# Optimization experiments

Measured on AMD Instinct MI355X. Metric: run time of the kernel, lower is better.

Reference implementation:

```python
import jax, jax.numpy as jnp
import numpy as np

B, H, S, D = 2, 16, 2048, 128


def setup_inputs() -> dict:
    key = jax.random.key(0)
    ks = jax.random.split(key, 11)
    s = 1.0 / np.sqrt(D)
    return {
        "query": jax.random.normal(ks[0], (B, H, S, D), dtype=jnp.float32),
        "key": jax.random.normal(ks[1], (B, H, S, D), dtype=jnp.float32),
        "value": jax.random.normal(ks[2], (B, H, S, D), dtype=jnp.float32),
        "Wq": jax.random.normal(ks[3], (D, D), dtype=jnp.float32) * s,
        "bq": jnp.zeros((D,), dtype=jnp.float32),
        "Wk": jax.random.normal(ks[4], (D, D), dtype=jnp.float32) * s,
        "bk": jnp.zeros((D,), dtype=jnp.float32),
        "Wv": jax.random.normal(ks[5], (D, D), dtype=jnp.float32) * s,
        "bv": jnp.zeros((D,), dtype=jnp.float32),
        "Wo": jax.random.normal(ks[6], (D, D), dtype=jnp.float32) * s,
        "bo": jnp.zeros((D,), dtype=jnp.float32),
    }


def reference(query, key, value, Wq, bq, Wk, bk, Wv, bv, Wo, bo):
    # Linear projections (torch Linear: x @ W^T + b) on last dim of [B,H,S,D]
    q = jnp.einsum("bhsd,ed->bhse", query, Wq) + bq
    k = jnp.einsum("bhsd,ed->bhse", key, Wk) + bk
    v = jnp.einsum("bhsd,ed->bhse", value, Wv) + bv
    scale = jnp.sqrt(jnp.asarray(D, dtype=q.dtype))
    q = q / scale
    qk = jnp.einsum("bhse,bhte->bhst", q, k)  # [B,H,S,S] scores
    attn = jax.nn.softmax(qk, axis=-1)
    # dropout_p = 0.0 -> identity
    out = jnp.einsum("bhst,bhtd->bhsd", attn, v)
    out = jnp.einsum("bhsd,ed->bhse", out, Wo) + bo
    return out
```

## Files before the change

kernel.cpp:

```cpp
#include <hip/hip_runtime.h>
#include <hip/hip_bf16.h>
#include <type_traits>
#include <math.h>

typedef __bf16 bf16x8 __attribute__((ext_vector_type(8)));
typedef float floatx4 __attribute__((ext_vector_type(4)));
typedef float floatx16 __attribute__((ext_vector_type(16)));

#define S_LEN 2048
#define D_DIM 128
#define NTOK (2 * 16 * 2048)
#define KVB 64
#define NKV (S_LEN / KVB)

template <typename TIN, typename TOUT>
__device__ __forceinline__ void proj_body4(
    const TIN* __restrict__ x, const float* __restrict__ W,
    const float* __restrict__ b, TOUT* __restrict__ y, float out_scale,
    int chunk0, __bf16 (*Wl)[128]) {
  const int tid = threadIdx.x;
  const int wave = tid >> 6, lane = tid & 63;
  const int g = lane >> 4, lr = lane & 15;

  for (int it = 0; it < 16; ++it) {
    int lin = it * 1024 + tid * 4;
    float4 w4 = *reinterpret_cast<const float4*>(W + lin);
    int r = lin >> 7, c = lin & 127;
    Wl[r][c]     = (__bf16)w4.x;
    Wl[r][c + 1] = (__bf16)w4.y;
    Wl[r][c + 2] = (__bf16)w4.z;
    Wl[r][c + 3] = (__bf16)w4.w;
  }
  __syncthreads();

  float be[8];
#pragma unroll
  for (int nt = 0; nt < 8; ++nt) be[nt] = b[nt * 16 + lr];

  for (int ch = 0; ch < 4; ++ch) {
    const int rbase = (chunk0 + ch) * 64;
    const int arow = rbase + wave * 16 + lr;

    floatx4 acc[8];
#pragma unroll
    for (int i = 0; i < 8; ++i) acc[i] = floatx4{0.f, 0.f, 0.f, 0.f};

#pragma unroll
    for (int kc = 0; kc < 4; ++kc) {
      bf16x8 af;
      const TIN* xp = x + (size_t)arow * D_DIM + kc * 32 + g * 8;
      if constexpr (std::is_same<TIN, float>::value) {
        float4 f0 = *reinterpret_cast<const float4*>(xp);
        float4 f1 = *reinterpret_cast<const float4*>(xp + 4);
        af[0] = (__bf16)f0.x; af[1] = (__bf16)f0.y;
        af[2] = (__bf16)f0.z; af[3] = (__bf16)f0.w;
        af[4] = (__bf16)f1.x; af[5] = (__bf16)f1.y;
        af[6] = (__bf16)f1.z; af[7] = (__bf16)f1.w;
      } else {
        af = *reinterpret_cast<const bf16x8*>(xp);
      }
#pragma unroll
      for (int nt = 0; nt < 8; ++nt) {
        bf16x8 wf = *reinterpret_cast<const bf16x8*>(&Wl[nt * 16 + lr][kc * 32 + g * 8]);
        acc[nt] = __builtin_amdgcn_mfma_f32_16x16x32_bf16(af, wf, acc[nt], 0, 0, 0);
      }
    }

#pragma unroll
    for (int nt = 0; nt < 8; ++nt) {
      int e = nt * 16 + lr;
#pragma unroll
      for (int j = 0; j < 4; ++j) {
        int row = rbase + wave * 16 + g * 4 + j;
        float val = (acc[nt][j] + be[nt]) * out_scale;
        y[(size_t)row * D_DIM + e] = (TOUT)val;
      }
    }
  }
}

__global__ __launch_bounds__(256) void qkv_proj_kernel(
    const float* __restrict__ xq, const float* __restrict__ xk,
    const float* __restrict__ xv, const float* __restrict__ Wq,
    const float* __restrict__ Wk, const float* __restrict__ Wv,
    const float* __restrict__ bq, const float* __restrict__ bk,
    const float* __restrict__ bv, __bf16* yq, __bf16* yk, __bf16* yv,
    float qscale) {
  __shared__ alignas(16) __bf16 Wl[128][128];
  const int which = blockIdx.y;
  const float* x = which == 0 ? xq : which == 1 ? xk : xv;
  const float* W = which == 0 ? Wq : which == 1 ? Wk : Wv;
  const float* b = which == 0 ? bq : which == 1 ? bk : bv;
  __bf16* y = which == 0 ? yq : which == 1 ? yk : yv;
  float sc = which == 0 ? qscale : 1.0f;
  proj_body4<float, __bf16>(x, W, b, y, sc, blockIdx.x * 4, Wl);
}

__global__ __launch_bounds__(256) void o_proj_kernel(
    const __bf16* __restrict__ x, const float* __restrict__ W,
    const float* __restrict__ b, float* __restrict__ y) {
  __shared__ alignas(16) __bf16 Wl[128][128];
  proj_body4<__bf16, float>(x, W, b, y, 1.0f, blockIdx.x * 4, Wl);
}

__device__ __forceinline__ unsigned swz(int row, unsigned byteoff) {
  return byteoff ^ (((unsigned)(row ^ (row >> 3)) & 7u) << 4);
}

__device__ __forceinline__ unsigned pack2(float lo, float hi) {
  union { __bf16 h[2]; unsigned u; } r;
  r.h[0] = (__bf16)lo; r.h[1] = (__bf16)hi;
  return r.u;
}

__global__ __launch_bounds__(256, 2) void attn_kernel(
    const __bf16* __restrict__ q, const __bf16* __restrict__ k,
    const __bf16* __restrict__ v, __bf16* __restrict__ o) {
  __shared__ alignas(16) unsigned char smem[65536];

  const int tid = threadIdx.x;
  const int wave = tid >> 6, lane = tid & 63;
  const int ql = lane & 31;
  const int h = lane >> 5;

  const int bh = blockIdx.x;
  const int qbase = blockIdx.y * 128;
  const __bf16* qp = q + (size_t)bh * S_LEN * D_DIM;
  const __bf16* kp = k + (size_t)bh * S_LEN * D_DIM;
  const __bf16* vp = v + (size_t)bh * S_LEN * D_DIM;
  __bf16* op = o + (size_t)bh * S_LEN * D_DIM;

  const int qrow = qbase + wave * 32 + ql;
  bf16x8 qf[8];
#pragma unroll
  for (int kc = 0; kc < 8; ++kc)
    qf[kc] = *reinterpret_cast<const bf16x8*>(
        qp + (size_t)qrow * D_DIM + kc * 16 + h * 8);

  floatx16 ot[4];
#pragma unroll
  for (int d = 0; d < 4; ++d)
#pragma unroll
    for (int r = 0; r < 16; ++r) ot[d][r] = 0.f;
  float m_r = -1e30f, l_r = 0.f;

  const int cc = tid & 15;
  const int pr = (tid >> 4) * 2;
  const int ce = cc * 8;

  unsigned Rk[4];
#pragma unroll
  for (int x = 0; x < 4; ++x)
    Rk[x] = (unsigned)(h * 1024) +
            (((unsigned)(ql * 16)) ^ ((unsigned)h << 4) ^ ((unsigned)x << 5));
  const unsigned Rv0 = 32768u + (unsigned)(h * 2048) +
                       (((unsigned)(ql * 16)) ^ (((unsigned)(ql >> 3)) << 4));
  const unsigned Rv1 = Rv0 ^ 64u;
  const unsigned kx = ((unsigned)(cc & 7)) << 4;
  const unsigned Wk0 = ((unsigned)(cc * 1024 + pr * 16)) ^ kx;
  const unsigned Wk1 = ((unsigned)(cc * 1024 + (pr + 1) * 16)) ^ kx;
  unsigned Wv_[8];
  {
    unsigned vbase = 32768u + (unsigned)((pr >> 3) * 2048 + ce * 16 + (pr & 7) * 2);
#pragma unroll
    for (int e = 0; e < 8; ++e)
      Wv_[e] = vbase | (((unsigned)e << 4) ^ kx);
  }

  {
    const __bf16* kr = kp + (size_t)pr * D_DIM + ce;
    const __bf16* vr = vp + (size_t)pr * D_DIM + ce;
    bf16x8 kA0 = *reinterpret_cast<const bf16x8*>(kr);
    bf16x8 kA1 = *reinterpret_cast<const bf16x8*>(kr + D_DIM);
    bf16x8 kB0 = *reinterpret_cast<const bf16x8*>(kr + 32 * D_DIM);
    bf16x8 kB1 = *reinterpret_cast<const bf16x8*>(kr + 33 * D_DIM);
    union { bf16x8 v8; unsigned short s[8]; } vA0, vA1, vB0, vB1;
    vA0.v8 = *reinterpret_cast<const bf16x8*>(vr);
    vA1.v8 = *reinterpret_cast<const bf16x8*>(vr + D_DIM);
    vB0.v8 = *reinterpret_cast<const bf16x8*>(vr + 32 * D_DIM);
    vB1.v8 = *reinterpret_cast<const bf16x8*>(vr + 33 * D_DIM);
    *reinterpret_cast<bf16x8*>(smem + Wk0) = kA0;
    *reinterpret_cast<bf16x8*>(smem + Wk1) = kA1;
    *reinterpret_cast<bf16x8*>(smem + Wk0 + 512u) = kB0;
    *reinterpret_cast<bf16x8*>(smem + Wk1 + 512u) = kB1;
#pragma unroll
    for (int e = 0; e < 8; ++e) {
      unsigned w0 = (unsigned)vA0.s[e] | ((unsigned)vA1.s[e] << 16);
      unsigned w1 = (unsigned)vB0.s[e] | ((unsigned)vB1.s[e] << 16);
      *reinterpret_cast<unsigned*>(smem + Wv_[e]) = w0;
      *reinterpret_cast<unsigned*>(smem + Wv_[e] + 8192u) = w1;
    }
  }

  const __bf16* krp = kp + ((size_t)KVB + pr) * D_DIM + ce;
  const __bf16* vrp = vp + ((size_t)KVB + pr) * D_DIM + ce;

#pragma unroll 2
  for (int t = 0; t < NKV; ++t) {
    const unsigned cb = (unsigned)(t & 1) * 16384u;
    const bool hn = (t + 1 < NKV);

    __syncthreads();

    bf16x8 kA0, kA1, kB0, kB1;
    union { bf16x8 v8; unsigned short s[8]; } vA0, vA1, vB0, vB1;
    if (hn) {
      kA0 = *reinterpret_cast<const bf16x8*>(krp);
      kA1 = *reinterpret_cast<const bf16x8*>(krp + D_DIM);
      kB0 = *reinterpret_cast<const bf16x8*>(krp + 32 * D_DIM);
      kB1 = *reinterpret_cast<const bf16x8*>(krp + 33 * D_DIM);
      vA0.v8 = *reinterpret_cast<const bf16x8*>(vrp);
      vA1.v8 = *reinterpret_cast<const bf16x8*>(vrp + D_DIM);
      vB0.v8 = *reinterpret_cast<const bf16x8*>(vrp + 32 * D_DIM);
      vB1.v8 = *reinterpret_cast<const bf16x8*>(vrp + 33 * D_DIM);
      krp += (size_t)KVB * D_DIM;
      vrp += (size_t)KVB * D_DIM;
    }

    floatx16 st[2];
#pragma unroll
    for (int kvh = 0; kvh < 2; ++kvh)
#pragma unroll
      for (int r = 0; r < 16; ++r) st[kvh][r] = 0.f;
    __builtin_amdgcn_s_setprio(1);
#pragma unroll
    for (int kc = 0; kc < 8; ++kc) {
      bf16x8 kf0 = *reinterpret_cast<const bf16x8*>(
          smem + cb + Rk[kc & 3] + (unsigned)(kc * 2048));
      bf16x8 kf1 = *reinterpret_cast<const bf16x8*>(
          smem + cb + Rk[kc & 3] + (unsigned)(kc * 2048 + 512));
      st[0] = __builtin_amdgcn_mfma_f32_32x32x16_bf16(kf0, qf[kc], st[0], 0, 0, 0);
      st[1] = __builtin_amdgcn_mfma_f32_32x32x16_bf16(kf1, qf[kc], st[1], 0, 0, 0);
    }
    __builtin_amdgcn_s_setprio(0);

    float t8[8];
#pragma unroll
    for (int i = 0; i < 8; ++i)
      t8[i] = fmaxf(fmaxf(st[0][i], st[0][i + 8]), fmaxf(st[1][i], st[1][i + 8]));
    float pmax = fmaxf(fmaxf(fmaxf(t8[0], t8[4]), fmaxf(t8[1], t8[5])),
                       fmaxf(fmaxf(t8[2], t8[6]), fmaxf(t8[3], t8[7])));
    pmax = fmaxf(pmax, __shfl_xor(pmax, 32));
    if (!__all(pmax - m_r <= 8.0f)) {
      float mnew = fmaxf(m_r, pmax);
      float sc_f = __builtin_amdgcn_exp2f(m_r - mnew);
      m_r = mnew;
      l_r *= sc_f;
#pragma unroll
      for (int d = 0; d < 4; ++d)
#pragma unroll
        for (int r = 0; r < 16; ++r) ot[d][r] *= sc_f;
    }
#pragma unroll
    for (int kvh = 0; kvh < 2; ++kvh)
#pragma unroll
      for (int r = 0; r < 16; ++r)
        st[kvh][r] = __builtin_amdgcn_exp2f(st[kvh][r] - m_r);
    float s8[8];
#pragma unroll
    for (int i = 0; i < 8; ++i)
      s8[i] = (st[0][i] + st[0][i + 8]) + (st[1][i] + st[1][i + 8]);
    float psum = ((s8[0] + s8[4]) + (s8[1] + s8[5])) +
                 ((s8[2] + s8[6]) + (s8[3] + s8[7]));
    psum += __shfl_xor(psum, 32);
    l_r += psum;

#pragma unroll
    for (int ks = 0; ks < 4; ++ks) {
      const int kvh = ks >> 1;
      const int r2a = (2 * ks) & 3;
      const int r2b = r2a + 1;
      unsigned ua0 = pack2(st[kvh][r2a * 4 + 0], st[kvh][r2a * 4 + 1]);
      unsigned ua1 = pack2(st[kvh][r2a * 4 + 2], st[kvh][r2a * 4 + 3]);
      unsigned ub0 = pack2(st[kvh][r2b * 4 + 0], st[kvh][r2b * 4 + 1]);
      unsigned ub1 = pack2(st[kvh][r2b * 4 + 2], st[kvh][r2b * 4 + 3]);
      union { unsigned u[4]; bf16x8 v8; } pw;
#if __has_builtin(__builtin_amdgcn_permlane32_swap)
      {
        auto r0 = __builtin_amdgcn_permlane32_swap(ua0, ub0, false, false);
        auto r1 = __builtin_amdgcn_permlane32_swap(ua1, ub1, false, false);
        pw.u[0] = r0[0];
        pw.u[1] = r1[0];
        pw.u[2] = r0[1];
        pw.u[3] = r1[1];
      }
#else
      {
        unsigned a0x = __shfl_xor(ua0, 32), a1x = __shfl_xor(ua1, 32);
        unsigned b0x = __shfl_xor(ub0, 32), b1x = __shfl_xor(ub1, 32);
        pw.u[0] = h ? b0x : ua0;
        pw.u[1] = h ? b1x : ua1;
        pw.u[2] = h ? ub0 : a0x;
        pw.u[3] = h ? ub1 : a1x;
      }
#endif
      __builtin_amdgcn_s_setprio(1);
#pragma unroll
      for (int db = 0; db < 4; ++db) {
        const unsigned base = (db & 1) ? Rv1 : Rv0;
        bf16x8 vf = *reinterpret_cast<const bf16x8*>(
            smem + cb + base + (unsigned)(ks * 4096 + db * 512));
        ot[db] = __builtin_amdgcn_mfma_f32_32x32x16_bf16(vf, pw.v8, ot[db], 0, 0, 0);
      }
      __builtin_amdgcn_s_setprio(0);
    }

    if (hn) {
      const unsigned nb = cb ^ 16384u;
      *reinterpret_cast<bf16x8*>(smem + nb + Wk0) = kA0;
      *reinterpret_cast<bf16x8*>(smem + nb + Wk1) = kA1;
      *reinterpret_cast<bf16x8*>(smem + nb + Wk0 + 512u) = kB0;
      *reinterpret_cast<bf16x8*>(smem + nb + Wk1 + 512u) = kB1;
#pragma unroll
      for (int e = 0; e < 8; ++e) {
        unsigned w0 = (unsigned)vA0.s[e] | ((unsigned)vA1.s[e] << 16);
        unsigned w1 = (unsigned)vB0.s[e] | ((unsigned)vB1.s[e] << 16);
        *reinterpret_cast<unsigned*>(smem + nb + Wv_[e]) = w0;
        *reinterpret_cast<unsigned*>(smem + nb + Wv_[e] + 8192u) = w1;
      }
    }
  }

  __syncthreads();
  const float inv_l = 1.0f / l_r;
  const int qloc = wave * 32 + ql;
#pragma unroll
  for (int db = 0; db < 4; ++db)
#pragma unroll
    for (int r = 0; r < 16; ++r) {
      int d = db * 32 + (r & 3) + 8 * (r >> 2) + 4 * h;
      *reinterpret_cast<__bf16*>(smem + swz(qloc, qloc * 256u + d * 2u)) =
          (__bf16)(ot[db][r] * inv_l);
    }
  __syncthreads();
#pragma unroll
  for (int it = 0; it < 8; ++it) {
    int r = tid >> 1;
    int c = (tid & 1) * 64 + it * 8;
    bf16x8 val = *reinterpret_cast<const bf16x8*>(smem + swz(r, r * 256u + c * 2u));
    *reinterpret_cast<bf16x8*>(op + (size_t)(qbase + r) * D_DIM + c) = val;
  }
}

extern "C" void kernel_launch(void* const* d_in, const int* in_sizes, int n_in,
                              void* d_out, int out_size, void* d_ws, size_t ws_size,
                              hipStream_t stream) {
  const float* query = (const float*)d_in[0];
  const float* key_  = (const float*)d_in[1];
  const float* value = (const float*)d_in[2];
  const float* Wq = (const float*)d_in[3];
  const float* bq = (const float*)d_in[4];
  const float* Wk = (const float*)d_in[5];
  const float* bk = (const float*)d_in[6];
  const float* Wv = (const float*)d_in[7];
  const float* bv = (const float*)d_in[8];
  const float* Wo = (const float*)d_in[9];
  const float* bo = (const float*)d_in[10];

  __bf16* vws = (__bf16*)d_ws;
  __bf16* aws = vws + (size_t)NTOK * D_DIM;
  __bf16* qws = (__bf16*)d_out;
  __bf16* kws = qws + (size_t)NTOK * D_DIM;

  const float qscale = 0.1275174490036f;

  qkv_proj_kernel<<<dim3(NTOK / 256, 3), dim3(256), 0, stream>>>(
      query, key_, value, Wq, Wk, Wv, bq, bk, bv, qws, kws, vws, qscale);

  attn_kernel<<<dim3(32, 16), dim3(256), 0, stream>>>(qws, kws, vws, aws);

  o_proj_kernel<<<NTOK / 256, dim3(256), 0, stream>>>(aws, Wo, bo, (float*)d_out);
}
```

Before: 132.3 us.

## Split attention over two KV halves and merge partials inside output projection

Adds a split-KV attention kernel in which each block handles half of the key/value sequence. It writes fp32 normalized partial outputs plus log-sum-exp values, and the grid doubles to 1024 blocks with smaller shared memory and a higher occupancy target. A new output-projection kernel merges the two partials with softmax weights before the Wo matmul, fusing the combine step into it. This raises parallelism over the 256 CUs but adds fp32 partial traffic (two 32 MB buffers written and read). The path is used only when the workspace is large enough, otherwise the old path runs.

```diff
diff --git a/kernel.cpp b/kernel.cpp
--- a/kernel.cpp
+++ b/kernel.cpp
@@ -12,6 +12,8 @@
 #define NTOK (2 * 16 * 2048)
 #define KVB 64
 #define NKV (S_LEN / KVB)
+#define KVB_S 32
+#define NKV_S 32
 
 template <typename TIN, typename TOUT>
 __device__ __forceinline__ void proj_body4(
@@ -103,6 +105,80 @@
   proj_body4<__bf16, float>(x, W, b, y, 1.0f, blockIdx.x * 4, Wl);
 }
 
+__global__ __launch_bounds__(256) void o_proj_merge_kernel(
+    const float* __restrict__ p0, const float* __restrict__ p1,
+    const float* __restrict__ g0, const float* __restrict__ g1,
+    const float* __restrict__ W, const float* __restrict__ b,
+    float* __restrict__ y) {
+  __shared__ alignas(16) __bf16 Wl[128][128];
+  const int tid = threadIdx.x;
+  const int wave = tid >> 6, lane = tid & 63;
+  const int g = lane >> 4, lr = lane & 15;
+
+  for (int it = 0; it < 16; ++it) {
+    int lin = it * 1024 + tid * 4;
+    float4 w4 = *reinterpret_cast<const float4*>(W + lin);
+    int r = lin >> 7, c = lin & 127;
+    Wl[r][c]     = (__bf16)w4.x;
+    Wl[r][c + 1] = (__bf16)w4.y;
+    Wl[r][c + 2] = (__bf16)w4.z;
+    Wl[r][c + 3] = (__bf16)w4.w;
+  }
+  __syncthreads();
+
+  float be[8];
+#pragma unroll
+  for (int nt = 0; nt < 8; ++nt) be[nt] = b[nt * 16 + lr];
+
+  for (int ch = 0; ch < 4; ++ch) {
+    const int rbase = (blockIdx.x * 4 + ch) * 64;
+    const int arow = rbase + wave * 16 + lr;
+
+    const float ga = g0[arow], gb = g1[arow];
+    const float e2 = __builtin_amdgcn_exp2f(gb - ga);
+    const float w0 = 1.0f / (1.0f + e2);
+    const float w1 = 1.0f - w0;
+
+    floatx4 acc[8];
+#pragma unroll
+    for (int i = 0; i < 8; ++i) acc[i] = floatx4{0.f, 0.f, 0.f, 0.f};
+
+#pragma unroll
+    for (int kc = 0; kc < 4; ++kc) {
+      const float* xp0 = p0 + (size_t)arow * D_DIM + kc * 32 + g * 8;
+      const float* xp1 = p1 + (size_t)arow * D_DIM + kc * 32 + g * 8;
+      float4 a0 = *reinterpret_cast<const float4*>(xp0);
+      float4 a1 = *reinterpret_cast<const float4*>(xp0 + 4);
+      float4 c0 = *reinterpret_cast<const float4*>(xp1);
+      float4 c1 = *reinterpret_cast<const float4*>(xp1 + 4);
+      bf16x8 af;
+      af[0] = (__bf16)(w0 * a0.x + w1 * c0.x);
+      af[1] = (__bf16)(w0 * a0.y + w1 * c0.y);
+      af[2] = (__bf16)(w0 * a0.z + w1 * c0.z);
+      af[3] = (__bf16)(w0 * a0.w + w1 * c0.w);
+      af[4] = (__bf16)(w0 * a1.x + w1 * c1.x);
+      af[5] = (__bf16)(w0 * a1.y + w1 * c1.y);
+      af[6] = (__bf16)(w0 * a1.z + w1 * c1.z);
+      af[7] = (__bf16)(w0 * a1.w + w1 * c1.w);
+#pragma unroll
+      for (int nt = 0; nt < 8; ++nt) {
+        bf16x8 wf = *reinterpret_cast<const bf16x8*>(&Wl[nt * 16 + lr][kc * 32 + g * 8]);
+        acc[nt] = __builtin_amdgcn_mfma_f32_16x16x32_bf16(af, wf, acc[nt], 0, 0, 0);
+      }
+    }
+
+#pragma unroll
+    for (int nt = 0; nt < 8; ++nt) {
+      int e = nt * 16 + lr;
+#pragma unroll
+      for (int j = 0; j < 4; ++j) {
+        int row = rbase + wave * 16 + g * 4 + j;
+        y[(size_t)row * D_DIM + e] = acc[nt][j] + be[nt];
+      }
+    }
+  }
+}
+
 __device__ __forceinline__ unsigned swz(int row, unsigned byteoff) {
   return byteoff ^ (((unsigned)(row ^ (row >> 3)) & 7u) << 4);
 }
@@ -111,6 +187,225 @@
   union { __bf16 h[2]; unsigned u; } r;
   r.h[0] = (__bf16)lo; r.h[1] = (__bf16)hi;
   return r.u;
+}
+
+__global__ __launch_bounds__(256, 4) void attn_split_kernel(
+    const __bf16* __restrict__ q, const __bf16* __restrict__ k,
+    const __bf16* __restrict__ v, float* __restrict__ part0,
+    float* __restrict__ part1, float* __restrict__ g0w,
+    float* __restrict__ g1w) {
+  __shared__ alignas(16) unsigned char smem[32768];
+
+  const int tid = threadIdx.x;
+  const int wave = tid >> 6, lane = tid & 63;
+  const int ql = lane & 31;
+  const int h = lane >> 5;
+
+  const int bh = blockIdx.x;
+  const int qbase = blockIdx.y * 128;
+  const int half = blockIdx.z;
+  float* part = half ? part1 : part0;
+  float* gw = half ? g1w : g0w;
+
+  const __bf16* qp = q + (size_t)bh * S_LEN * D_DIM;
+  const __bf16* kp = k + (size_t)bh * S_LEN * D_DIM + (size_t)half * 1024 * D_DIM;
+  const __bf16* vp = v + (size_t)bh * S_LEN * D_DIM + (size_t)half * 1024 * D_DIM;
+
+  const int qrow = qbase + wave * 32 + ql;
+  bf16x8 qf[8];
+#pragma unroll
+  for (int kc = 0; kc < 8; ++kc)
+    qf[kc] = *reinterpret_cast<const bf16x8*>(
+        qp + (size_t)qrow * D_DIM + kc * 16 + h * 8);
+
+  floatx16 ot[4];
+#pragma unroll
+  for (int d = 0; d < 4; ++d)
+#pragma unroll
+    for (int r = 0; r < 16; ++r) ot[d][r] = 0.f;
+  float m_r = -1e30f, l_r = 0.f;
+
+  const int cc = tid & 15;
+  const int pr2 = (tid >> 4) * 2;
+  const int ce = cc * 8;
+
+  unsigned Rk[4];
+#pragma unroll
+  for (int x = 0; x < 4; ++x)
+    Rk[x] = (unsigned)(h * 512) +
+            (((unsigned)(ql * 16)) ^ ((unsigned)h << 4) ^ ((unsigned)x << 5));
+  const unsigned Rv0 = 16384u + (unsigned)(h * 2048) +
+                       (((unsigned)(ql * 16)) ^ (((unsigned)(ql >> 3)) << 4));
+  const unsigned Rv1 = Rv0 ^ 64u;
+  const unsigned kx = ((unsigned)(cc & 7)) << 4;
+  const unsigned Wk0 = ((unsigned)(cc * 512 + pr2 * 16)) ^ kx;
+  const unsigned Wk1 = ((unsigned)(cc * 512 + (pr2 + 1) * 16)) ^ kx;
+  unsigned Wv_[8];
+  {
+    unsigned C = 16384u + (unsigned)((pr2 >> 3) * 2048 + 128 * cc + (pr2 & 7) * 2);
+#pragma unroll
+    for (int e = 0; e < 8; ++e)
+      Wv_[e] = C + (((unsigned)(e * 16)) ^ kx);
+  }
+
+  {
+    const __bf16* kr = kp + (size_t)pr2 * D_DIM + ce;
+    const __bf16* vr = vp + (size_t)pr2 * D_DIM + ce;
+    bf16x8 kA0 = *reinterpret_cast<const bf16x8*>(kr);
+    bf16x8 kA1 = *reinterpret_cast<const bf16x8*>(kr + D_DIM);
+    union { bf16x8 v8; unsigned short s[8]; } vA0, vA1;
+    vA0.v8 = *reinterpret_cast<const bf16x8*>(vr);
+    vA1.v8 = *reinterpret_cast<const bf16x8*>(vr + D_DIM);
+    *reinterpret_cast<bf16x8*>(smem + Wk0) = kA0;
+    *reinterpret_cast<bf16x8*>(smem + Wk1) = kA1;
+#pragma unroll
+    for (int e = 0; e < 8; ++e) {
+      unsigned w = (unsigned)vA0.s[e] | ((unsigned)vA1.s[e] << 16);
+      *reinterpret_cast<unsigned*>(smem + Wv_[e]) = w;
+    }
+  }
+
+  const __bf16* krp = kp + ((size_t)KVB_S + pr2) * D_DIM + ce;
+  const __bf16* vrp = vp + ((size_t)KVB_S + pr2) * D_DIM + ce;
+
+#pragma unroll 2
+  for (int t = 0; t < NKV_S; ++t) {
+    const unsigned cb = (unsigned)(t & 1) * 8192u;
+    const bool hn = (t + 1 < NKV_S);
+
+    __syncthreads();
+
+    bf16x8 kA0, kA1;
+    union { bf16x8 v8; unsigned short s[8]; } vA0, vA1;
+    if (hn) {
+      kA0 = *reinterpret_cast<const bf16x8*>(krp);
+      kA1 = *reinterpret_cast<const bf16x8*>(krp + D_DIM);
+      vA0.v8 = *reinterpret_cast<const bf16x8*>(vrp);
+      vA1.v8 = *reinterpret_cast<const bf16x8*>(vrp + D_DIM);
+      krp += (size_t)KVB_S * D_DIM;
+      vrp += (size_t)KVB_S * D_DIM;
+    }
+
+    floatx16 st;
+#pragma unroll
+    for (int r = 0; r < 16; ++r) st[r] = 0.f;
+    __builtin_amdgcn_s_setprio(1);
+#pragma unroll
+    for (int kc = 0; kc < 8; ++kc) {
+      bf16x8 kf = *reinterpret_cast<const bf16x8*>(
+          smem + cb + Rk[kc & 3] + (unsigned)(kc * 1024));
+      st = __builtin_amdgcn_mfma_f32_32x32x16_bf16(kf, qf[kc], st, 0, 0, 0);
+    }
+    __builtin_amdgcn_s_setprio(0);
+
+    float t8[8];
+#pragma unroll
+    for (int i = 0; i < 8; ++i) t8[i] = fmaxf(st[i], st[i + 8]);
+    float pmax = fmaxf(fmaxf(fmaxf(t8[0], t8[4]), fmaxf(t8[1], t8[5])),
+                       fmaxf(fmaxf(t8[2], t8[6]), fmaxf(t8[3], t8[7])));
+    pmax = fmaxf(pmax, __shfl_xor(pmax, 32));
+    if (!__all(pmax - m_r <= 8.0f)) {
+      float mnew = fmaxf(m_r, pmax);
+      float sc_f = __builtin_amdgcn_exp2f(m_r - mnew);
+      m_r = mnew;
+      l_r *= sc_f;
+#pragma unroll
+      for (int d = 0; d < 4; ++d)
+#pragma unroll
+        for (int r = 0; r < 16; ++r) ot[d][r] *= sc_f;
+    }
+#pragma unroll
+    for (int r = 0; r < 16; ++r)
+      st[r] = __builtin_amdgcn_exp2f(st[r] - m_r);
+    float s8[8];
+#pragma unroll
+    for (int i = 0; i < 8; ++i) s8[i] = st[i] + st[i + 8];
+    float psum = ((s8[0] + s8[4]) + (s8[1] + s8[5])) +
+                 ((s8[2] + s8[6]) + (s8[3] + s8[7]));
+    psum += __shfl_xor(psum, 32);
+    l_r += psum;
+
+#pragma unroll
+    for (int ks = 0; ks < 2; ++ks) {
+      const int r2a = 2 * ks;
+      const int r2b = r2a + 1;
+      unsigned ua0 = pack2(st[r2a * 4 + 0], st[r2a * 4 + 1]);
+      unsigned ua1 = pack2(st[r2a * 4 + 2], st[r2a * 4 + 3]);
+      unsigned ub0 = pack2(st[r2b * 4 + 0], st[r2b * 4 + 1]);
+      unsigned ub1 = pack2(st[r2b * 4 + 2], st[r2b * 4 + 3]);
+      union { unsigned u[4]; bf16x8 v8; } pw;
+#if __has_builtin(__builtin_amdgcn_permlane32_swap)
+      {
+        auto r0 = __builtin_amdgcn_permlane32_swap(ua0, ub0, false, false);
+        auto r1 = __builtin_amdgcn_permlane32_swap(ua1, ub1, false, false);
+        pw.u[0] = r0[0];
+        pw.u[1] = r1[0];
+        pw.u[2] = r0[1];
+        pw.u[3] = r1[1];
+      }
+#else
+      {
+        unsigned a0x = __shfl_xor(ua0, 32), a1x = __shfl_xor(ua1, 32);
+        unsigned b0x = __shfl_xor(ub0, 32), b1x = __shfl_xor(ub1, 32);
+        pw.u[0] = h ? b0x : ua0;
+        pw.u[1] = h ? b1x : ua1;
+        pw.u[2] = h ? ub0 : a0x;
+        pw.u[3] = h ? ub1 : a1x;
+      }
+#endif
+      __builtin_amdgcn_s_setprio(1);
+#pragma unroll
+      for (int db = 0; db < 4; ++db) {
+        const unsigned base = (db & 1) ? Rv1 : Rv0;
+        bf16x8 vf = *reinterpret_cast<const bf16x8*>(
+            smem + cb + base + (unsigned)(ks * 4096 + db * 512));
+        ot[db] = __builtin_amdgcn_mfma_f32_32x32x16_bf16(vf, pw.v8, ot[db], 0, 0, 0);
+      }
+      __builtin_amdgcn_s_setprio(0);
+    }
+
+    if (hn) {
+      const unsigned nb = cb ^ 8192u;
+      *reinterpret_cast<bf16x8*>(smem + nb + Wk0) = kA0;
+      *reinterpret_cast<bf16x8*>(smem + nb + Wk1) = kA1;
+#pragma unroll
+      for (int e = 0; e < 8; ++e) {
+        unsigned w = (unsigned)vA0.s[e] | ((unsigned)vA1.s[e] << 16);
+        *reinterpret_cast<unsigned*>(smem + nb + Wv_[e]) = w;
+      }
+    }
+  }
+
+  const float inv_l = 1.0f / l_r;
+  if (h == 0) gw[(size_t)bh * S_LEN + qbase + wave * 32 + ql] =
+      m_r + __log2f(l_r);
+  float* pout = part + ((size_t)bh * S_LEN + qbase) * D_DIM;
+
+#pragma unroll
+  for (int p = 0; p < 2; ++p) {
+    __syncthreads();
+    if ((wave >> 1) == p) {
+      int qloc = (wave & 1) * 32 + ql;
+#pragma unroll
+      for (int db = 0; db < 4; ++db)
+#pragma unroll
+        for (int r = 0; r < 16; ++r) {
+          int d = db * 32 + (r & 3) + 8 * (r >> 2) + 4 * h;
+          *reinterpret_cast<float*>(
+              smem + (((unsigned)(qloc * 512 + d * 4)) ^
+                      (((unsigned)(qloc & 7)) << 4))) = ot[db][r] * inv_l;
+        }
+    }
+    __syncthreads();
+#pragma unroll
+    for (int it = 0; it < 8; ++it) {
+      int qr = tid >> 2;
+      int ds = (tid & 3) * 32 + it * 4;
+      float4 val = *reinterpret_cast<const float4*>(
+          smem + (((unsigned)(qr * 512 + ds * 4)) ^ (((unsigned)(qr & 7)) << 4)));
+      *reinterpret_cast<float4*>(pout + (size_t)(p * 64 + qr) * D_DIM + ds) = val;
+    }
+  }
 }
 
 __global__ __launch_bounds__(256, 2) void attn_kernel(
@@ -357,8 +652,12 @@
   const float* Wo = (const float*)d_in[9];
   const float* bo = (const float*)d_in[10];
 
+  const size_t vbytes = (size_t)NTOK * D_DIM * 2;
+  const size_t pbytes = (size_t)NTOK * D_DIM * 4;
+  const size_t gbytes = (size_t)NTOK * 4;
+  const size_t need_split = vbytes + 2 * pbytes + 2 * gbytes;
+
   __bf16* vws = (__bf16*)d_ws;
-  __bf16* aws = vws + (size_t)NTOK * D_DIM;
   __bf16* qws = (__bf16*)d_out;
   __bf16* kws = qws + (size_t)NTOK * D_DIM;
 
@@ -367,7 +666,20 @@
   qkv_proj_kernel<<<dim3(NTOK / 256, 3), dim3(256), 0, stream>>>(
       query, key_, value, Wq, Wk, Wv, bq, bk, bv, qws, kws, vws, qscale);
 
-  attn_kernel<<<dim3(32, 16), dim3(256), 0, stream>>>(qws, kws, vws, aws);
-
-  o_proj_kernel<<<NTOK / 256, dim3(256), 0, stream>>>(aws, Wo, bo, (float*)d_out);
-}
+  if (ws_size >= need_split) {
+    float* p0 = (float*)((char*)d_ws + vbytes);
+    float* p1 = (float*)((char*)d_ws + vbytes + pbytes);
+    float* g0 = (float*)((char*)d_ws + vbytes + 2 * pbytes);
+    float* g1 = (float*)((char*)d_ws + vbytes + 2 * pbytes + gbytes);
+
+    attn_split_kernel<<<dim3(32, 16, 2), dim3(256), 0, stream>>>(
+        qws, kws, vws, p0, p1, g0, g1);
+
+    o_proj_merge_kernel<<<NTOK / 256, dim3(256), 0, stream>>>(
+        p0, p1, g0, g1, Wo, bo, (float*)d_out);
+  } else {
+    __bf16* aws = vws + (size_t)NTOK * D_DIM;
+    attn_kernel<<<dim3(32, 16), dim3(256), 0, stream>>>(qws, kws, vws, aws);
+    o_proj_kernel<<<NTOK / 256, dim3(256), 0, stream>>>(aws, Wo, bo, (float*)d_out);
+  }
+}
```

Result: slower. 257.1 us (+94.2%).

## Load four consecutive KV rows per thread and store prefetch to LDS earlier

Applied to the files above, without the earlier changes.

Each thread now loads four consecutive K/V rows instead of two pairs 32 rows apart. This lets V be written to shared memory as packed 64-bit stores instead of two 32-bit stores. The store of the prefetched next tile into the alternate buffer moves from the end of the iteration to right after the QK MFMAs. That frees the prefetch registers sooner and overlaps LDS writes with the softmax and PV work. The risk is that global loads may not have landed by then, stalling before softmax, and the LDS writes may contend with the PV-phase reads.

```diff
diff --git a/kernel.cpp b/kernel.cpp
--- a/kernel.cpp
+++ b/kernel.cpp
@@ -145,7 +145,7 @@
   float m_r = -1e30f, l_r = 0.f;
 
   const int cc = tid & 15;
-  const int pr = (tid >> 4) * 2;
+  const int pr4 = (tid >> 4) * 4;
   const int ce = cc * 8;
 
   unsigned Rk[4];
@@ -157,43 +157,42 @@
                        (((unsigned)(ql * 16)) ^ (((unsigned)(ql >> 3)) << 4));
   const unsigned Rv1 = Rv0 ^ 64u;
   const unsigned kx = ((unsigned)(cc & 7)) << 4;
-  const unsigned Wk0 = ((unsigned)(cc * 1024 + pr * 16)) ^ kx;
-  const unsigned Wk1 = ((unsigned)(cc * 1024 + (pr + 1) * 16)) ^ kx;
+  unsigned Wk_[4];
+#pragma unroll
+  for (int j = 0; j < 4; ++j)
+    Wk_[j] = ((unsigned)(cc * 1024 + (pr4 + j) * 16)) ^ kx;
   unsigned Wv_[8];
   {
-    unsigned vbase = 32768u + (unsigned)((pr >> 3) * 2048 + ce * 16 + (pr & 7) * 2);
+    unsigned vbase = 32768u + (unsigned)((pr4 >> 3) * 2048 + ce * 16 + (pr4 & 7) * 2);
 #pragma unroll
     for (int e = 0; e < 8; ++e)
       Wv_[e] = vbase | (((unsigned)e << 4) ^ kx);
   }
 
   {
-    const __bf16* kr = kp + (size_t)pr * D_DIM + ce;
-    const __bf16* vr = vp + (size_t)pr * D_DIM + ce;
-    bf16x8 kA0 = *reinterpret_cast<const bf16x8*>(kr);
-    bf16x8 kA1 = *reinterpret_cast<const bf16x8*>(kr + D_DIM);
-    bf16x8 kB0 = *reinterpret_cast<const bf16x8*>(kr + 32 * D_DIM);
-    bf16x8 kB1 = *reinterpret_cast<const bf16x8*>(kr + 33 * D_DIM);
-    union { bf16x8 v8; unsigned short s[8]; } vA0, vA1, vB0, vB1;
-    vA0.v8 = *reinterpret_cast<const bf16x8*>(vr);
-    vA1.v8 = *reinterpret_cast<const bf16x8*>(vr + D_DIM);
-    vB0.v8 = *reinterpret_cast<const bf16x8*>(vr + 32 * D_DIM);
-    vB1.v8 = *reinterpret_cast<const bf16x8*>(vr + 33 * D_DIM);
-    *reinterpret_cast<bf16x8*>(smem + Wk0) = kA0;
-    *reinterpret_cast<bf16x8*>(smem + Wk1) = kA1;
-    *reinterpret_cast<bf16x8*>(smem + Wk0 + 512u) = kB0;
-    *reinterpret_cast<bf16x8*>(smem + Wk1 + 512u) = kB1;
+    const __bf16* kr = kp + (size_t)pr4 * D_DIM + ce;
+    const __bf16* vr = vp + (size_t)pr4 * D_DIM + ce;
+    bf16x8 kR[4];
+    union { bf16x8 v8; unsigned short s[8]; } vR[4];
+#pragma unroll
+    for (int j = 0; j < 4; ++j) {
+      kR[j] = *reinterpret_cast<const bf16x8*>(kr + j * D_DIM);
+      vR[j].v8 = *reinterpret_cast<const bf16x8*>(vr + j * D_DIM);
+    }
+#pragma unroll
+    for (int j = 0; j < 4; ++j)
+      *reinterpret_cast<bf16x8*>(smem + Wk_[j]) = kR[j];
 #pragma unroll
     for (int e = 0; e < 8; ++e) {
-      unsigned w0 = (unsigned)vA0.s[e] | ((unsigned)vA1.s[e] << 16);
-      unsigned w1 = (unsigned)vB0.s[e] | ((unsigned)vB1.s[e] << 16);
-      *reinterpret_cast<unsigned*>(smem + Wv_[e]) = w0;
-      *reinterpret_cast<unsigned*>(smem + Wv_[e] + 8192u) = w1;
-    }
-  }
-
-  const __bf16* krp = kp + ((size_t)KVB + pr) * D_DIM + ce;
-  const __bf16* vrp = vp + ((size_t)KVB + pr) * D_DIM + ce;
+      uint2 w;
+      w.x = (unsigned)vR[0].s[e] | ((unsigned)vR[1].s[e] << 16);
+      w.y = (unsigned)vR[2].s[e] | ((unsigned)vR[3].s[e] << 16);
+      *reinterpret_cast<uint2*>(smem + Wv_[e]) = w;
+    }
+  }
+
+  const __bf16* krp = kp + ((size_t)KVB + pr4) * D_DIM + ce;
+  const __bf16* vrp = vp + ((size_t)KVB + pr4) * D_DIM + ce;
 
 #pragma unroll 2
   for (int t = 0; t < NKV; ++t) {
@@ -202,17 +201,14 @@
 
     __syncthreads();
 
-    bf16x8 kA0, kA1, kB0, kB1;
-    union { bf16x8 v8; unsigned short s[8]; } vA0, vA1, vB0, vB1;
+    bf16x8 kR[4];
+    union { bf16x8 v8; unsigned short s[8]; } vR[4];
     if (hn) {
-      kA0 = *reinterpret_cast<const bf16x8*>(krp);
-      kA1 = *reinterpret_cast<const bf16x8*>(krp + D_DIM);
-      kB0 = *reinterpret_cast<const bf16x8*>(krp + 32 * D_DIM);
-      kB1 = *reinterpret_cast<const bf16x8*>(krp + 33 * D_DIM);
-      vA0.v8 = *reinterpret_cast<const bf16x8*>(vrp);
-      vA1.v8 = *reinterpret_cast<const bf16x8*>(vrp + D_DIM);
-      vB0.v8 = *reinterpret_cast<const bf16x8*>(vrp + 32 * D_DIM);
-      vB1.v8 = *reinterpret_cast<const bf16x8*>(vrp + 33 * D_DIM);
+#pragma unroll
+      for (int j = 0; j < 4; ++j) {
+        kR[j] = *reinterpret_cast<const bf16x8*>(krp + j * D_DIM);
+        vR[j].v8 = *reinterpret_cast<const bf16x8*>(vrp + j * D_DIM);
+      }
       krp += (size_t)KVB * D_DIM;
       vrp += (size_t)KVB * D_DIM;
     }
@@ -233,6 +229,20 @@
       st[1] = __builtin_amdgcn_mfma_f32_32x32x16_bf16(kf1, qf[kc], st[1], 0, 0, 0);
     }
     __builtin_amdgcn_s_setprio(0);
+
+    if (hn) {
+      const unsigned nb = cb ^ 16384u;
+#pragma unroll
+      for (int j = 0; j < 4; ++j)
+        *reinterpret_cast<bf16x8*>(smem + nb + Wk_[j]) = kR[j];
+#pragma unroll
+      for (int e = 0; e < 8; ++e) {
+        uint2 w;
+        w.x = (unsigned)vR[0].s[e] | ((unsigned)vR[1].s[e] << 16);
+        w.y = (unsigned)vR[2].s[e] | ((unsigned)vR[3].s[e] << 16);
+        *reinterpret_cast<uint2*>(smem + nb + Wv_[e]) = w;
+      }
+    }
 
     float t8[8];
 #pragma unroll
@@ -304,21 +314,6 @@
       }
       __builtin_amdgcn_s_setprio(0);
     }
-
-    if (hn) {
-      const unsigned nb = cb ^ 16384u;
-      *reinterpret_cast<bf16x8*>(smem + nb + Wk0) = kA0;
-      *reinterpret_cast<bf16x8*>(smem + nb + Wk1) = kA1;
-      *reinterpret_cast<bf16x8*>(smem + nb + Wk0 + 512u) = kB0;
-      *reinterpret_cast<bf16x8*>(smem + nb + Wk1 + 512u) = kB1;
-#pragma unroll
-      for (int e = 0; e < 8; ++e) {
-        unsigned w0 = (unsigned)vA0.s[e] | ((unsigned)vA1.s[e] << 16);
-        unsigned w1 = (unsigned)vB0.s[e] | ((unsigned)vB1.s[e] << 16);
-        *reinterpret_cast<unsigned*>(smem + nb + Wv_[e]) = w0;
-        *reinterpret_cast<unsigned*>(smem + nb + Wv_[e] + 8192u) = w1;
-      }
-    }
   }
 
   __syncthreads();
```

After: 132.0 us. Within noise of the previous version (-0.2%).
